# Optimization experiments

Measured on AMD Instinct MI355X. Metric: run time of the kernel, lower is better.

## Reference

```python
import jax, jax.numpy as jnp
import numpy as np

TAU = 2.0      # tau_thr in the source
EPS = 1e-5     # BatchNorm1d default eps
ALPHA = 8.0    # ATan surrogate alpha


@jax.custom_vjp
def atan_spike(x):
    # Heaviside forward, ATan surrogate backward (spikingjelly surrogate.ATan)
    return (x >= 0.0).astype(x.dtype)

def _as_fwd(x):
    return atan_spike(x), x

def _as_bwd(x, g):
    sg = (ALPHA / 2.0) / (1.0 + (jnp.pi / 2.0 * ALPHA * x) ** 2)
    return (g * sg,)

atan_spike.defvjp(_as_fwd, _as_bwd)


def lif(x, thr=1.0):
    # Multi-step LIFNode: v <- v + (x - v)/tau ; spike = H(v - thr);
    # hard reset to v_reset=0 with detach_reset=True.
    def step(v, xt):
        v = v + (xt - v) / TAU
        s = atan_spike(v - thr)
        v = v * (1.0 - jax.lax.stop_gradient(s))
        return v, s
    _, s = jax.lax.scan(step, jnp.zeros_like(x[0]), x)
    return s


def bn(x, p):
    # inference BatchNorm1d over channel dim C of [T,B,C,N]; p = [gamma,beta,mean,var] each [C]
    g, b, m, v = p
    inv = g / jnp.sqrt(v + EPS)
    return x * inv[:, None] + (b - m * inv)[:, None]


def setup_inputs() -> dict:
    key = jax.random.key(0)
    ks = jax.random.split(key, 11)
    T, B, C, H, W = 4, 64, 384, 14, 14
    sc = C ** -0.5
    x = jax.random.normal(ks[0], (T, B, C, H, W), jnp.float32)
    q_w = jax.random.normal(ks[1], (C, C), jnp.float32) * sc
    k_w = jax.random.normal(ks[2], (C, C), jnp.float32) * sc
    v_w = jax.random.normal(ks[3], (C, C), jnp.float32) * sc
    proj_w = jax.random.normal(ks[4], (C, C), jnp.float32) * sc
    proj_b = jax.random.normal(ks[5], (C,), jnp.float32) * 0.02
    def bn_params(k):
        return jax.random.uniform(k, (4, C), jnp.float32, 0.1, 1.0)
    return {
        'x': x, 'q_w': q_w, 'k_w': k_w, 'v_w': v_w,
        'proj_w': proj_w, 'proj_b': proj_b,
        'q_bn_p': bn_params(ks[6]), 'k_bn_p': bn_params(ks[7]),
        'v_bn_p': bn_params(ks[8]), 'p_bn_p': bn_params(ks[9]),
    }


def reference(x, q_w, k_w, v_w, proj_w, proj_b, q_bn_p, k_bn_p, v_bn_p, p_bn_p):
    T, B, C, H, W = x.shape
    nh = 8
    d = C // nh
    N = H * W
    identity = x

    xs = lif(x).reshape(T, B, C, N)  # binary spikes [T,B,C,N]

    def branch(w, p):
        # conv1x1 (C->C) + BN + LIF, then split heads -> [T,B,h,N,d]
        y = bn(jnp.einsum('tbcn,dc->tbdn', xs, w), p)
        s = lif(y)
        return s.reshape(T, B, nh, d, N).transpose(0, 1, 2, 4, 3)

    q = branch(q_w, q_bn_p)
    k = branch(k_w, k_bn_p)
    v = branch(v_w, v_bn_p)

    # unnormalized binary attention (no softmax)
    attn = jnp.einsum('tbhnd,tbhmd->tbhnm', q, k)      # [T,B,h,N,N]
    y = jnp.einsum('tbhnm,tbhmd->tbhnd', attn, v) * 0.125

    y = y.transpose(0, 1, 2, 4, 3).reshape(T, B, C, N)  # merge heads back to C
    y = lif(y, thr=0.5)                                 # attn_lif, v_threshold=0.5

    y = jnp.einsum('tbcn,dc->tbdn', y, proj_w) + proj_b[:, None]
    y = bn(y, p_bn_p)
    return y.reshape(T, B, C, H, W) + identity
```

## Files before the change

kernel.cpp:

```cpp
#include <hip/hip_runtime.h>
#include <hip/hip_bf16.h>

typedef unsigned short u16;
typedef unsigned char  u8;
typedef unsigned int   u32;
typedef unsigned long long u64;
typedef __attribute__((ext_vector_type(8))) short  short8;
typedef __attribute__((ext_vector_type(8))) __bf16 bf16x8;
typedef __attribute__((ext_vector_type(4))) float  f32x4;
typedef __attribute__((ext_vector_type(4))) int    i32x4;

#define DI static __device__ __forceinline__

constexpr int T_ = 4, B_ = 64, C_ = 384, N_ = 196, NH_ = 8, DH_ = 48;
constexpr int J1_ = B_ * N_;
constexpr int J_  = T_ * J1_;
constexpr int K2_ = 2 * C_;
constexpr int M1_ = 3 * C_;

DI u16 f2bf(float x){ __hip_bfloat16 h = __float2bfloat16(x); u16 u; __builtin_memcpy(&u,&h,2); return u; }
DI float bf2f(u16 u){ __hip_bfloat16 h; __builtin_memcpy(&h,&u,2); return __bfloat162float(h); }

DI void gload16(const void* g, void* lds){
  __builtin_amdgcn_global_load_lds((const __attribute__((address_space(1))) u32*)g,
                                   (__attribute__((address_space(3))) u32*)lds, 16, 0, 0);
}
DI bf16x8 ldbf8(const u16* p){ short8 v = *(const short8*)p; return __builtin_bit_cast(bf16x8, v); }
DI int SWZ(int n){ return ((n >> 3) ^ (n >> 5)) & 3; }

__global__ __launch_bounds__(256) void k0_prep(
    const float* __restrict__ qw, const float* __restrict__ kw,
    const float* __restrict__ vw, const float* __restrict__ pw,
    const float* __restrict__ qbn, const float* __restrict__ kbn,
    const float* __restrict__ vbn, const float* __restrict__ pbn,
    u16* __restrict__ A2f, u16* __restrict__ A2pf,
    float* __restrict__ invq, float* __restrict__ betaq,
    float* __restrict__ invp, float* __restrict__ betap)
{
  int id = blockIdx.x * 256 + threadIdx.x;
  const int nAf = M1_ * K2_;
  const int nPf = C_ * K2_;
  if (id < nAf) {
    int tmp = id;
    int e    = tmp & 7;  tmp >>= 3;
    int lane = tmp & 63; tmp >>= 6;
    int ks2  = tmp & 1;  tmp >>= 1;
    int mt   = tmp & 3;  tmp >>= 2;
    int wm   = tmp & 1;  tmp >>= 1;
    int kt   = tmp % 12;
    int bm   = tmp / 12;
    int cc = bm*128 + wm*64 + mt*16 + (lane & 15);
    int k  = kt*64 + ks2*32 + (lane >> 4)*8 + e;
    int br = cc / C_, row = cc % C_;
    const float* w = (br == 0) ? qw : ((br == 1) ? kw : vw);
    float wv = w[row * C_ + (k < C_ ? k : k - C_)];
    u16 hi = f2bf(wv);
    A2f[id] = (k < C_) ? hi : f2bf(__fsub_rn(wv, bf2f(hi)));
  } else if (id < nAf + nPf) {
    int tmp = id - nAf;
    int id2 = tmp;
    int e    = tmp & 7;  tmp >>= 3;
    int lane = tmp & 63; tmp >>= 6;
    int ks2  = tmp & 1;  tmp >>= 1;
    int mt   = tmp & 3;  tmp >>= 2;
    int wm   = tmp & 1;  tmp >>= 1;
    int kt   = tmp % 12;
    int bm   = tmp / 12;
    int cc = bm*128 + wm*64 + mt*16 + (lane & 15);
    int k  = kt*64 + ks2*32 + (lane >> 4)*8 + e;
    float wv = pw[cc * C_ + (k < C_ ? k : k - C_)];
    u16 hi = f2bf(wv);
    A2pf[id2] = (k < C_) ? hi : f2bf(__fsub_rn(wv, bf2f(hi)));
  } else if (id < nAf + nPf + M1_) {
    int c = id - nAf - nPf;
    int br = c / C_, cr = c % C_;
    const float* p = (br == 0) ? qbn : ((br == 1) ? kbn : vbn);
    float g = p[cr], bb = p[C_ + cr], mm = p[2*C_ + cr], vv = p[3*C_ + cr];
    float inv = g / sqrtf(__fadd_rn(vv, 1e-5f));
    invq[c] = inv; betaq[c] = __fsub_rn(bb, __fmul_rn(mm, inv));
  } else if (id < nAf + nPf + M1_ + C_) {
    int c = id - nAf - nPf - M1_;
    float g = pbn[c], bb = pbn[C_ + c], mm = pbn[2*C_ + c], vv = pbn[3*C_ + c];
    float inv = g / sqrtf(__fadd_rn(vv, 1e-5f));
    invp[c] = inv; betap[c] = __fsub_rn(bb, __fmul_rn(mm, inv));
  }
}

__global__ __launch_bounds__(256) void k1_lif_x(const float* __restrict__ x, u16* __restrict__ xs_t)
{
  int b = blockIdx.x / 12, ch = blockIdx.x % 12;
  int c0 = ch * 32;
  __shared__ u16 sp[4 * 32 * 200];
  int tid = threadIdx.x;
  for (int idx = tid; idx < 32 * 49; idx += 256) {
    int ci = idx / 49, n4 = idx % 49;
    float v0 = 0.f, v1 = 0.f, v2 = 0.f, v3 = 0.f;
    for (int t = 0; t < 4; t++) {
      const float4 xv = *reinterpret_cast<const float4*>(
          &x[((size_t)((t*B_ + b)*C_ + c0 + ci))*N_ + n4*4]);
      u16 s0, s1, s2, s3;
      v0 = __fadd_rn(v0, __fmul_rn(__fsub_rn(xv.x, v0), 0.5f)); { bool s = (v0 >= 1.0f); s0 = s ? (u16)0x3F80 : (u16)0; v0 = __fmul_rn(v0, s ? 0.f : 1.f); }
      v1 = __fadd_rn(v1, __fmul_rn(__fsub_rn(xv.y, v1), 0.5f)); { bool s = (v1 >= 1.0f); s1 = s ? (u16)0x3F80 : (u16)0; v1 = __fmul_rn(v1, s ? 0.f : 1.f); }
      v2 = __fadd_rn(v2, __fmul_rn(__fsub_rn(xv.z, v2), 0.5f)); { bool s = (v2 >= 1.0f); s2 = s ? (u16)0x3F80 : (u16)0; v2 = __fmul_rn(v2, s ? 0.f : 1.f); }
      v3 = __fadd_rn(v3, __fmul_rn(__fsub_rn(xv.w, v3), 0.5f)); { bool s = (v3 >= 1.0f); s3 = s ? (u16)0x3F80 : (u16)0; v3 = __fmul_rn(v3, s ? 0.f : 1.f); }
      u64 pk = (u64)s0 | ((u64)s1 << 16) | ((u64)s2 << 32) | ((u64)s3 << 48);
      *reinterpret_cast<u64*>(&sp[(t*32 + ci)*200 + n4*4]) = pk;
    }
  }
  __syncthreads();
  for (int idx = tid; idx < 4 * 8 * N_; idx += 256) {
    int ci4 = idx & 7; int q = idx >> 3; int n = q % N_; int t = q / N_;
    u16 a0 = sp[(t*32 + ci4*4 + 0)*200 + n];
    u16 a1 = sp[(t*32 + ci4*4 + 1)*200 + n];
    u16 a2 = sp[(t*32 + ci4*4 + 2)*200 + n];
    u16 a3 = sp[(t*32 + ci4*4 + 3)*200 + n];
    u64 pk = (u64)a0 | ((u64)a1 << 16) | ((u64)a2 << 32) | ((u64)a3 << 48);
    *reinterpret_cast<u64*>(&xs_t[((size_t)((t*B_ + b)*N_ + n))*C_ + c0 + ci4*4]) = pk;
  }
}

__global__ __launch_bounds__(256, 2) void g1_branch(
    const u16* __restrict__ A2f, const u16* __restrict__ xs_t,
    const float* __restrict__ invq, const float* __restrict__ betaq,
    u8* __restrict__ qs, u8* __restrict__ ks_, u8* __restrict__ vs)
{
  int blk = blockIdx.x;
  int grp = blk / 72, rem = blk % 72;
  int bm = rem >> 3;
  int jt = grp * 8 + (rem & 7);
  if (jt >= 98) return;
  int cc0 = bm * 128;
  int colb = jt * 128;

  __shared__ u16 Bt[128 * 64];

  int tid = threadIdx.x;
  int lane = tid & 63, w = tid >> 6;
  int lr = lane & 15, lg = lane >> 4;
  int rsw = lr & 7;
  int wm = w & 1;
  int mrow = wm * 64, ncol = (w >> 1) * 64;

  float vst[4][4][4];
  #pragma unroll
  for (int a = 0; a < 4; a++)
    #pragma unroll
    for (int bq = 0; bq < 4; bq++)
      #pragma unroll
      for (int r = 0; r < 4; r++) vst[a][bq][r] = 0.f;

  f32x4 acc[4][4];
  bf16x8 af[2][4];

  auto LOADA = [&](int kt2) {
    int wb = (bm * 12 + kt2) * 2 + wm;
    #pragma unroll
    for (int ks2 = 0; ks2 < 2; ks2++)
      #pragma unroll
      for (int mt = 0; mt < 4; mt++)
        af[ks2][mt] = ldbf8(A2f + ((size_t)(((wb * 4 + mt) * 2 + ks2) * 64) + lane) * 8);
  };

  LOADA(0);

  for (int u = 0; u < 48; u++) {
    int t = u / 12, kt = u - t * 12;
    int ckB0 = kt * 64;
    int ckB = (ckB0 >= C_) ? (ckB0 - C_) : ckB0;
    long j0 = (long)t * J1_ + colb;

    #pragma unroll
    for (int i = 0; i < 4; i++) {
      int L0 = tid + i * 256;
      int r = L0 >> 3;
      int c = (L0 & 7) ^ (r & 7);
      gload16(xs_t + (size_t)(j0 + r) * C_ + ckB + c * 8, &Bt[L0 * 8]);
    }

    if (kt == 0) {
      #pragma unroll
      for (int a = 0; a < 4; a++)
        #pragma unroll
        for (int bq = 0; bq < 4; bq++) acc[a][bq] = (f32x4){0.f, 0.f, 0.f, 0.f};
    }
    __syncthreads();

    #pragma unroll
    for (int ks2 = 0; ks2 < 2; ks2++) {
      bf16x8 bfr[4];
      #pragma unroll
      for (int nn = 0; nn < 4; nn++)
        bfr[nn] = ldbf8(&Bt[(ncol + nn*16 + lr)*64 + (((ks2*4 + lg) ^ rsw) * 8)]);
      #pragma unroll
      for (int mt = 0; mt < 4; mt++)
        #pragma unroll
        for (int nn = 0; nn < 4; nn++)
          acc[mt][nn] = __builtin_amdgcn_mfma_f32_16x16x32_bf16(af[ks2][mt], bfr[nn], acc[mt][nn], 0, 0, 0);
    }

    if (u + 1 < 48) {
      int un = u + 1;
      LOADA(un - (un / 12) * 12);
    }

    if (kt == 11) {
      #pragma unroll
      for (int mt = 0; mt < 4; mt++) {
        #pragma unroll
        for (int r = 0; r < 4; r++) {
          int cc = cc0 + mrow + mt*16 + lg*4 + r;
          float inv = invq[cc], beta = betaq[cc];
          int br = cc / C_, c = cc % C_;
          u8* dst = ((br == 0) ? qs : ((br == 1) ? ks_ : vs)) + (size_t)c * J_ + t * J1_ + colb;
          #pragma unroll
          for (int nn = 0; nn < 4; nn++) {
            int col = ncol + nn*16 + lr;
            float yb = __fadd_rn(__fmul_rn(acc[mt][nn][r], inv), beta);
            float v = vst[mt][nn][r];
            v = __fadd_rn(v, __fmul_rn(__fsub_rn(yb, v), 0.5f));
            bool sgl = (v >= 1.0f);
            vst[mt][nn][r] = __fmul_rn(v, sgl ? 0.f : 1.f);
            dst[col] = sgl ? (u8)1 : (u8)0;
          }
        }
      }
    }
    __syncthreads();
  }
}

__global__ __launch_bounds__(256) void k3_attn(
    const u8* __restrict__ qs, const u8* __restrict__ ks_, const u8* __restrict__ vs,
    u16* __restrict__ s2t)
{
  int b = blockIdx.x >> 3, h = blockIdx.x & 7;
  __shared__ __align__(16) signed char qL[208 * 80];
  __shared__ __align__(16) signed char kL[208 * 80];
  __shared__ __align__(16) signed char vL[48 * 272];
  __shared__ __align__(16) signed char aL[4 * 16 * 272];

  int tid = threadIdx.x, lane = tid & 63, w = tid >> 6;
  int lr = lane & 15, lg = lane >> 4;

  for (int i = tid; i < 208*80/4; i += 256) { ((int*)qL)[i] = 0; ((int*)kL)[i] = 0; }
  for (int i = tid; i < 48*272/4; i += 256) ((int*)vL)[i] = 0;
  for (int i = tid; i < 4*16*272/4; i += 256) ((int*)aL)[i] = 0;
  __syncthreads();

  float vst[4][3][4];
  #pragma unroll
  for (int a = 0; a < 4; a++)
    #pragma unroll
    for (int d = 0; d < 3; d++)
      #pragma unroll
      for (int r = 0; r < 4; r++) vst[a][d][r] = 0.f;

  signed char* arow = &aL[w * 16 * 272];
  const i32x4 zero4 = {0, 0, 0, 0};

  for (int t = 0; t < 4; t++) {
    size_t off = (size_t)(t*B_ + b) * N_;
    for (int i = tid; i < 588; i += 256) {
      int dd4 = i / 49, n4 = i - dd4 * 49;
      size_t rb = (size_t)(h*DH_ + dd4*4) * J_ + off + n4*4;
      u32 q0 = *(const u32*)(qs + rb);
      u32 q1 = *(const u32*)(qs + rb + J_);
      u32 q2 = *(const u32*)(qs + rb + 2*(size_t)J_);
      u32 q3 = *(const u32*)(qs + rb + 3*(size_t)J_);
      u32 k0 = *(const u32*)(ks_ + rb);
      u32 k1 = *(const u32*)(ks_ + rb + J_);
      u32 k2 = *(const u32*)(ks_ + rb + 2*(size_t)J_);
      u32 k3 = *(const u32*)(ks_ + rb + 3*(size_t)J_);
      u32 v0 = *(const u32*)(vs + rb);
      u32 v1 = *(const u32*)(vs + rb + J_);
      u32 v2 = *(const u32*)(vs + rb + 2*(size_t)J_);
      u32 v3 = *(const u32*)(vs + rb + 3*(size_t)J_);
      int c16 = dd4 >> 2, bb4 = (dd4 & 3) << 2;
      #pragma unroll
      for (int jj = 0; jj < 4; jj++) {
        u32 tq = ((q0 >> (8*jj)) & 0xFFu) | (((q1 >> (8*jj)) & 0xFFu) << 8)
               | (((q2 >> (8*jj)) & 0xFFu) << 16) | (((q3 >> (8*jj)) & 0xFFu) << 24);
        u32 tk = ((k0 >> (8*jj)) & 0xFFu) | (((k1 >> (8*jj)) & 0xFFu) << 8)
               | (((k2 >> (8*jj)) & 0xFFu) << 16) | (((k3 >> (8*jj)) & 0xFFu) << 24);
        int n = n4*4 + jj;
        int cs = ((c16 ^ SWZ(n)) << 4) + bb4;
        *(u32*)(qL + n*80 + cs) = tq;
        *(u32*)(kL + n*80 + cs) = tk;
      }
      *(u32*)(vL + (dd4*4 + 0)*272 + n4*4) = v0;
      *(u32*)(vL + (dd4*4 + 1)*272 + n4*4) = v1;
      *(u32*)(vL + (dd4*4 + 2)*272 + n4*4) = v2;
      *(u32*)(vL + (dd4*4 + 3)*272 + n4*4) = v3;
    }
    __syncthreads();

    int nslots = (w == 0) ? 4 : 3;
    for (int sl = 0; sl < nslots; sl++) {
      int ni = w + sl * 4;
      int nq = ni*16 + lr;
      i32x4 bq = *reinterpret_cast<const i32x4*>(qL + nq*80 + ((lg ^ SWZ(nq)) << 4));
      for (int mj = 0; mj < 13; mj++) {
        int mk = mj*16 + lr;
        i32x4 ak = *reinterpret_cast<const i32x4*>(kL + mk*80 + ((lg ^ SWZ(mk)) << 4));
        i32x4 d = __builtin_amdgcn_mfma_i32_16x16x64_i8(ak, bq, zero4, 0, 0, 0);
        u32 pk = (u32)d[0] | ((u32)d[1] << 8) | ((u32)d[2] << 16) | ((u32)d[3] << 24);
        *(u32*)(arow + lr*272 + mj*16 + lg*4) = pk;
      }
      #pragma unroll
      for (int di = 0; di < 3; di++) {
        i32x4 acc = zero4;
        #pragma unroll
        for (int ks2 = 0; ks2 < 4; ks2++) {
          i32x4 aa = *reinterpret_cast<const i32x4*>(arow + lr*272 + ks2*64 + lg*16);
          i32x4 bb = *reinterpret_cast<const i32x4*>(vL + (di*16 + lr)*272 + ks2*64 + lg*16);
          acc = __builtin_amdgcn_mfma_i32_16x16x64_i8(aa, bb, acc, 0, 0, 0);
        }
        #pragma unroll
        for (int r = 0; r < 4; r++) {
          int n = ni*16 + lg*4 + r;
          float xv = __fmul_rn((float)acc[r], 0.125f);
          float v = vst[sl][di][r];
          v = __fadd_rn(v, __fmul_rn(__fsub_rn(xv, v), 0.5f));
          bool s = (v >= 0.5f);
          vst[sl][di][r] = __fmul_rn(v, s ? 0.f : 1.f);
          if (n < N_)
            s2t[((size_t)((t*B_ + b)*N_ + n))*C_ + h*DH_ + di*16 + lr] = s ? (u16)0x3F80 : (u16)0;
        }
      }
    }
    __syncthreads();
  }
}

__global__ __launch_bounds__(256, 2) void g2_proj(
    const u16* __restrict__ A2pf, const u16* __restrict__ s2t,
    const float* __restrict__ invp, const float* __restrict__ betap,
    const float* __restrict__ pb, const float* __restrict__ x,
    float* __restrict__ out)
{
  int blk = blockIdx.x;
  int grp = blk / 24, rem = blk % 24;
  int bm = rem >> 3;
  int bn = grp * 8 + (rem & 7);
  int cc0 = bm * 128, j0 = bn * 128;

  __shared__ u16 Bt[128 * 64];

  int tid = threadIdx.x;
  int lane = tid & 63, w = tid >> 6;
  int lr = lane & 15, lg = lane >> 4;
  int rsw = lr & 7;
  int wm = w & 1;
  int mrow = wm * 64, ncol = (w >> 1) * 64;

  f32x4 acc[4][4];
  #pragma unroll
  for (int a = 0; a < 4; a++)
    #pragma unroll
    for (int bq = 0; bq < 4; bq++) acc[a][bq] = (f32x4){0.f, 0.f, 0.f, 0.f};

  bf16x8 af[2][4];
  auto LOADA = [&](int kt2) {
    int wb = (bm * 12 + kt2) * 2 + wm;
    #pragma unroll
    for (int ks2 = 0; ks2 < 2; ks2++)
      #pragma unroll
      for (int mt = 0; mt < 4; mt++)
        af[ks2][mt] = ldbf8(A2pf + ((size_t)(((wb * 4 + mt) * 2 + ks2) * 64) + lane) * 8);
  };

  LOADA(0);

  for (int kt = 0; kt < 12; kt++) {
    int ckB0 = kt * 64;
    int ckB = (ckB0 >= C_) ? (ckB0 - C_) : ckB0;
    #pragma unroll
    for (int i = 0; i < 4; i++) {
      int L0 = tid + i * 256;
      int r = L0 >> 3;
      int c = (L0 & 7) ^ (r & 7);
      gload16(s2t + (size_t)(j0 + r) * C_ + ckB + c * 8, &Bt[L0 * 8]);
    }
    __syncthreads();

    #pragma unroll
    for (int ks2 = 0; ks2 < 2; ks2++) {
      bf16x8 bfr[4];
      #pragma unroll
      for (int nn = 0; nn < 4; nn++)
        bfr[nn] = ldbf8(&Bt[(ncol + nn*16 + lr)*64 + (((ks2*4 + lg) ^ rsw) * 8)]);
      #pragma unroll
      for (int mt = 0; mt < 4; mt++)
        #pragma unroll
        for (int nn = 0; nn < 4; nn++)
          acc[mt][nn] = __builtin_amdgcn_mfma_f32_16x16x32_bf16(af[ks2][mt], bfr[nn], acc[mt][nn], 0, 0, 0);
    }

    if (kt < 11) LOADA(kt + 1);
    __syncthreads();
  }

  #pragma unroll
  for (int mt = 0; mt < 4; mt++) {
    #pragma unroll
    for (int r = 0; r < 4; r++) {
      int cc = cc0 + mrow + mt*16 + lg*4 + r;
      float inv = invp[cc], beta = betap[cc], pbv = pb[cc];
      #pragma unroll
      for (int nn = 0; nn < 4; nn++) {
        int j = j0 + ncol + nn*16 + lr;
        float y = __fadd_rn(acc[mt][nn][r], pbv);
        float o = __fadd_rn(__fmul_rn(y, inv), beta);
        int jq = j / N_, n = j % N_;
        size_t addr = ((size_t)jq * C_ + cc) * N_ + n;
        out[addr] = __fadd_rn(o, x[addr]);
      }
    }
  }
}

extern "C" void kernel_launch(void* const* d_in, const int* in_sizes, int n_in,
                              void* d_out, int out_size, void* d_ws, size_t ws_size,
                              hipStream_t stream)
{
  (void)in_sizes; (void)n_in; (void)out_size; (void)ws_size;
  const float* x   = (const float*)d_in[0];
  const float* qw  = (const float*)d_in[1];
  const float* kw  = (const float*)d_in[2];
  const float* vw  = (const float*)d_in[3];
  const float* pw  = (const float*)d_in[4];
  const float* pbv = (const float*)d_in[5];
  const float* qbn = (const float*)d_in[6];
  const float* kbn = (const float*)d_in[7];
  const float* vbn = (const float*)d_in[8];
  const float* pbn = (const float*)d_in[9];

  char* ws = (char*)d_ws;
  u16*   A2f   = (u16*)  (ws + 0);
  u16*   A2pf  = (u16*)  (ws + 1769472);
  float* invq  = (float*)(ws + 2359296);
  float* betaq = (float*)(ws + 2363904);
  float* invp  = (float*)(ws + 2368512);
  float* betap = (float*)(ws + 2370048);
  u16*   xs_t  = (u16*)  (ws + 2371584);
  u16*   s2t   = xs_t;
  u8*    qs    = (u8*)   (ws + 40906752);
  u8*    ks    = (u8*)   (ws + 60174336);
  u8*    vs    = (u8*)   (ws + 79441920);

  k0_prep<<<4614, 256, 0, stream>>>(qw, kw, vw, pw, qbn, kbn, vbn, pbn,
                                    A2f, A2pf, invq, betaq, invp, betap);
  k1_lif_x<<<768, 256, 0, stream>>>(x, xs_t);
  g1_branch<<<936, 256, 0, stream>>>(A2f, xs_t, invq, betaq, qs, ks, vs);
  k3_attn<<<512, 256, 0, stream>>>(qs, ks, vs, s2t);
  g2_proj<<<1176, 256, 0, stream>>>(A2pf, s2t, invp, betap, pbv, x, (float*)d_out);
}
```

Baseline: 294.1 us.

## Write Q/K spikes in per-head token-major layout and load MFMA fragments directly

The branch GEMM epilogue now writes Q and K spikes into a per-(t,b,head) page laid out token-major with 48 bytes per token, packing four channels per 32-bit store. The attention kernel then reads Q/K MFMA fragments straight from global memory instead of transposing and staging them through swizzled LDS, which removes that LDS staging pass and its transposition arithmetic. The prep kernel zero-fills the padding rows of each page. The cost is uncached global reads inside the inner attention loop and more prep work.

```diff
diff --git a/kernel.cpp b/kernel.cpp
--- a/kernel.cpp
+++ b/kernel.cpp
@@ -17,6 +17,7 @@
 constexpr int J_  = T_ * J1_;
 constexpr int K2_ = 2 * C_;
 constexpr int M1_ = 3 * C_;
+constexpr int PGE_ = 208 * 48;
 
 DI u16 f2bf(float x){ __hip_bfloat16 h = __float2bfloat16(x); u16 u; __builtin_memcpy(&u,&h,2); return u; }
 DI float bf2f(u16 u){ __hip_bfloat16 h; __builtin_memcpy(&h,&u,2); return __bfloat162float(h); }
@@ -26,7 +27,6 @@
                                    (__attribute__((address_space(3))) u32*)lds, 16, 0, 0);
 }
 DI bf16x8 ldbf8(const u16* p){ short8 v = *(const short8*)p; return __builtin_bit_cast(bf16x8, v); }
-DI int SWZ(int n){ return ((n >> 3) ^ (n >> 5)) & 3; }
 
 __global__ __launch_bounds__(256) void k0_prep(
     const float* __restrict__ qw, const float* __restrict__ kw,
@@ -35,11 +35,14 @@
     const float* __restrict__ vbn, const float* __restrict__ pbn,
     u16* __restrict__ A2f, u16* __restrict__ A2pf,
     float* __restrict__ invq, float* __restrict__ betaq,
-    float* __restrict__ invp, float* __restrict__ betap)
+    float* __restrict__ invp, float* __restrict__ betap,
+    u8* __restrict__ qt, u8* __restrict__ kt_)
 {
   int id = blockIdx.x * 256 + threadIdx.x;
   const int nAf = M1_ * K2_;
   const int nPf = C_ * K2_;
+  const int base1 = nAf + nPf + M1_ + C_;
+  const int nPad = 2048 * 144;
   if (id < nAf) {
     int tmp = id;
     int e    = tmp & 7;  tmp >>= 3;
@@ -78,11 +81,19 @@
     float g = p[cr], bb = p[C_ + cr], mm = p[2*C_ + cr], vv = p[3*C_ + cr];
     float inv = g / sqrtf(__fadd_rn(vv, 1e-5f));
     invq[c] = inv; betaq[c] = __fsub_rn(bb, __fmul_rn(mm, inv));
-  } else if (id < nAf + nPf + M1_ + C_) {
+  } else if (id < base1) {
     int c = id - nAf - nPf - M1_;
     float g = pbn[c], bb = pbn[C_ + c], mm = pbn[2*C_ + c], vv = pbn[3*C_ + c];
     float inv = g / sqrtf(__fadd_rn(vv, 1e-5f));
     invp[c] = inv; betap[c] = __fsub_rn(bb, __fmul_rn(mm, inv));
+  } else if (id < base1 + nPad) {
+    int id3 = id - base1;
+    int p = id3 / 144, rr = (id3 % 144) / 12, uu = id3 % 12;
+    *(u32*)(qt + (size_t)p * PGE_ + (196 + rr) * 48 + uu * 4) = 0u;
+  } else if (id < base1 + 2 * nPad) {
+    int id3 = id - base1 - nPad;
+    int p = id3 / 144, rr = (id3 % 144) / 12, uu = id3 % 12;
+    *(u32*)(kt_ + (size_t)p * PGE_ + (196 + rr) * 48 + uu * 4) = 0u;
   }
 }
 
@@ -122,7 +133,7 @@
 __global__ __launch_bounds__(256, 2) void g1_branch(
     const u16* __restrict__ A2f, const u16* __restrict__ xs_t,
     const float* __restrict__ invq, const float* __restrict__ betaq,
-    u8* __restrict__ qs, u8* __restrict__ ks_, u8* __restrict__ vs)
+    u8* __restrict__ qt, u8* __restrict__ kt_, u8* __restrict__ vs)
 {
   int blk = blockIdx.x;
   int grp = blk / 72, rem = blk % 72;
@@ -140,6 +151,7 @@
   int rsw = lr & 7;
   int wm = w & 1;
   int mrow = wm * 64, ncol = (w >> 1) * 64;
+  int brw = (cc0 + mrow) / C_;
 
   float vst[4][4][4];
   #pragma unroll
@@ -204,23 +216,53 @@
     }
 
     if (kt == 11) {
-      #pragma unroll
-      for (int mt = 0; mt < 4; mt++) {
-        #pragma unroll
-        for (int r = 0; r < 4; r++) {
-          int cc = cc0 + mrow + mt*16 + lg*4 + r;
-          float inv = invq[cc], beta = betaq[cc];
-          int br = cc / C_, c = cc % C_;
-          u8* dst = ((br == 0) ? qs : ((br == 1) ? ks_ : vs)) + (size_t)c * J_ + t * J1_ + colb;
+      if (brw == 2) {
+        #pragma unroll
+        for (int mt = 0; mt < 4; mt++) {
+          #pragma unroll
+          for (int r = 0; r < 4; r++) {
+            int cc = cc0 + mrow + mt*16 + lg*4 + r;
+            float inv = invq[cc], beta = betaq[cc];
+            int c = cc - 2 * C_;
+            u8* dst = vs + (size_t)c * J_ + t * J1_ + colb;
+            #pragma unroll
+            for (int nn = 0; nn < 4; nn++) {
+              int col = ncol + nn*16 + lr;
+              float yb = __fadd_rn(__fmul_rn(acc[mt][nn][r], inv), beta);
+              float v = vst[mt][nn][r];
+              v = __fadd_rn(v, __fmul_rn(__fsub_rn(yb, v), 0.5f));
+              bool sgl = (v >= 1.0f);
+              vst[mt][nn][r] = __fmul_rn(v, sgl ? 0.f : 1.f);
+              dst[col] = sgl ? (u8)1 : (u8)0;
+            }
+          }
+        }
+      } else {
+        u8* baseb = brw ? kt_ : qt;
+        #pragma unroll
+        for (int mt = 0; mt < 4; mt++) {
+          int ccb = cc0 + mrow + mt*16 + lg*4;
+          float invv[4], betav[4];
+          #pragma unroll
+          for (int r = 0; r < 4; r++) { invv[r] = invq[ccb + r]; betav[r] = betaq[ccb + r]; }
+          int c = ccb - brw * C_;
+          int h = c / DH_, dd0 = c % DH_;
           #pragma unroll
           for (int nn = 0; nn < 4; nn++) {
-            int col = ncol + nn*16 + lr;
-            float yb = __fadd_rn(__fmul_rn(acc[mt][nn][r], inv), beta);
-            float v = vst[mt][nn][r];
-            v = __fadd_rn(v, __fmul_rn(__fsub_rn(yb, v), 0.5f));
-            bool sgl = (v >= 1.0f);
-            vst[mt][nn][r] = __fmul_rn(v, sgl ? 0.f : 1.f);
-            dst[col] = sgl ? (u8)1 : (u8)0;
+            int col = colb + ncol + nn*16 + lr;
+            u32 bidx = ((u32)col * 85599u) >> 24;
+            int n = col - (int)bidx * 196;
+            u32 pk = 0;
+            #pragma unroll
+            for (int r = 0; r < 4; r++) {
+              float yb = __fadd_rn(__fmul_rn(acc[mt][nn][r], invv[r]), betav[r]);
+              float v = vst[mt][nn][r];
+              v = __fadd_rn(v, __fmul_rn(__fsub_rn(yb, v), 0.5f));
+              bool sgl = (v >= 1.0f);
+              vst[mt][nn][r] = __fmul_rn(v, sgl ? 0.f : 1.f);
+              pk |= (sgl ? 1u : 0u) << (8 * r);
+            }
+            *(u32*)(baseb + (size_t)((t*B_ + (int)bidx)*NH_ + h) * PGE_ + n*48 + dd0) = pk;
           }
         }
       }
@@ -230,20 +272,17 @@
 }
 
 __global__ __launch_bounds__(256) void k3_attn(
-    const u8* __restrict__ qs, const u8* __restrict__ ks_, const u8* __restrict__ vs,
+    const u8* __restrict__ qt, const u8* __restrict__ kt_, const u8* __restrict__ vs,
     u16* __restrict__ s2t)
 {
   int b = blockIdx.x >> 3, h = blockIdx.x & 7;
-  __shared__ __align__(16) signed char qL[208 * 80];
-  __shared__ __align__(16) signed char kL[208 * 80];
-  __shared__ __align__(16) signed char vL[48 * 272];
+  __shared__ __align__(16) signed char vL[48 * 304];
   __shared__ __align__(16) signed char aL[4 * 16 * 272];
 
   int tid = threadIdx.x, lane = tid & 63, w = tid >> 6;
   int lr = lane & 15, lg = lane >> 4;
 
-  for (int i = tid; i < 208*80/4; i += 256) { ((int*)qL)[i] = 0; ((int*)kL)[i] = 0; }
-  for (int i = tid; i < 48*272/4; i += 256) ((int*)vL)[i] = 0;
+  for (int i = tid; i < 48*304/4; i += 256) ((int*)vL)[i] = 0;
   for (int i = tid; i < 4*16*272/4; i += 256) ((int*)aL)[i] = 0;
   __syncthreads();
 
@@ -260,49 +299,25 @@
 
   for (int t = 0; t < 4; t++) {
     size_t off = (size_t)(t*B_ + b) * N_;
-    for (int i = tid; i < 588; i += 256) {
-      int dd4 = i / 49, n4 = i - dd4 * 49;
-      size_t rb = (size_t)(h*DH_ + dd4*4) * J_ + off + n4*4;
-      u32 q0 = *(const u32*)(qs + rb);
-      u32 q1 = *(const u32*)(qs + rb + J_);
-      u32 q2 = *(const u32*)(qs + rb + 2*(size_t)J_);
-      u32 q3 = *(const u32*)(qs + rb + 3*(size_t)J_);
-      u32 k0 = *(const u32*)(ks_ + rb);
-      u32 k1 = *(const u32*)(ks_ + rb + J_);
-      u32 k2 = *(const u32*)(ks_ + rb + 2*(size_t)J_);
-      u32 k3 = *(const u32*)(ks_ + rb + 3*(size_t)J_);
-      u32 v0 = *(const u32*)(vs + rb);
-      u32 v1 = *(const u32*)(vs + rb + J_);
-      u32 v2 = *(const u32*)(vs + rb + 2*(size_t)J_);
-      u32 v3 = *(const u32*)(vs + rb + 3*(size_t)J_);
-      int c16 = dd4 >> 2, bb4 = (dd4 & 3) << 2;
-      #pragma unroll
-      for (int jj = 0; jj < 4; jj++) {
-        u32 tq = ((q0 >> (8*jj)) & 0xFFu) | (((q1 >> (8*jj)) & 0xFFu) << 8)
-               | (((q2 >> (8*jj)) & 0xFFu) << 16) | (((q3 >> (8*jj)) & 0xFFu) << 24);
-        u32 tk = ((k0 >> (8*jj)) & 0xFFu) | (((k1 >> (8*jj)) & 0xFFu) << 8)
-               | (((k2 >> (8*jj)) & 0xFFu) << 16) | (((k3 >> (8*jj)) & 0xFFu) << 24);
-        int n = n4*4 + jj;
-        int cs = ((c16 ^ SWZ(n)) << 4) + bb4;
-        *(u32*)(qL + n*80 + cs) = tq;
-        *(u32*)(kL + n*80 + cs) = tk;
-      }
-      *(u32*)(vL + (dd4*4 + 0)*272 + n4*4) = v0;
-      *(u32*)(vL + (dd4*4 + 1)*272 + n4*4) = v1;
-      *(u32*)(vL + (dd4*4 + 2)*272 + n4*4) = v2;
-      *(u32*)(vL + (dd4*4 + 3)*272 + n4*4) = v3;
-    }
-    __syncthreads();
-
+    for (int i = tid; i < 48 * 49; i += 256) {
+      int dd = i / 49, n4 = i - dd * 49;
+      u32 vv = *(const u32*)(vs + (size_t)(h*DH_ + dd) * J_ + off + n4*4);
+      *(u32*)(vL + dd*304 + n4*4) = vv;
+    }
+    __syncthreads();
+
+    size_t pb = (size_t)((t*B_ + b)*NH_ + h) * PGE_;
     int nslots = (w == 0) ? 4 : 3;
     for (int sl = 0; sl < nslots; sl++) {
       int ni = w + sl * 4;
       int nq = ni*16 + lr;
-      i32x4 bq = *reinterpret_cast<const i32x4*>(qL + nq*80 + ((lg ^ SWZ(nq)) << 4));
+      i32x4 afr = zero4;
+      if (lg < 3) afr = *reinterpret_cast<const i32x4*>(qt + pb + (size_t)nq*48 + lg*16);
       for (int mj = 0; mj < 13; mj++) {
         int mk = mj*16 + lr;
-        i32x4 ak = *reinterpret_cast<const i32x4*>(kL + mk*80 + ((lg ^ SWZ(mk)) << 4));
-        i32x4 d = __builtin_amdgcn_mfma_i32_16x16x64_i8(ak, bq, zero4, 0, 0, 0);
+        i32x4 ak = zero4;
+        if (lg < 3) ak = *reinterpret_cast<const i32x4*>(kt_ + pb + (size_t)mk*48 + lg*16);
+        i32x4 d = __builtin_amdgcn_mfma_i32_16x16x64_i8(ak, afr, zero4, 0, 0, 0);
         u32 pk = (u32)d[0] | ((u32)d[1] << 8) | ((u32)d[2] << 16) | ((u32)d[3] << 24);
         *(u32*)(arow + lr*272 + mj*16 + lg*4) = pk;
       }
@@ -312,7 +327,7 @@
         #pragma unroll
         for (int ks2 = 0; ks2 < 4; ks2++) {
           i32x4 aa = *reinterpret_cast<const i32x4*>(arow + lr*272 + ks2*64 + lg*16);
-          i32x4 bb = *reinterpret_cast<const i32x4*>(vL + (di*16 + lr)*272 + ks2*64 + lg*16);
+          i32x4 bb = *reinterpret_cast<const i32x4*>(vL + (di*16 + lr)*304 + ks2*64 + lg*16);
           acc = __builtin_amdgcn_mfma_i32_16x16x64_i8(aa, bb, acc, 0, 0, 0);
         }
         #pragma unroll
@@ -444,14 +459,14 @@
   float* betap = (float*)(ws + 2370048);
   u16*   xs_t  = (u16*)  (ws + 2371584);
   u16*   s2t   = xs_t;
-  u8*    qs    = (u8*)   (ws + 40906752);
-  u8*    ks    = (u8*)   (ws + 60174336);
-  u8*    vs    = (u8*)   (ws + 79441920);
-
-  k0_prep<<<4614, 256, 0, stream>>>(qw, kw, vw, pw, qbn, kbn, vbn, pbn,
-                                    A2f, A2pf, invq, betaq, invp, betap);
+  u8*    qt    = (u8*)   (ws + 40906752);
+  u8*    kt_   = (u8*)   (ws + 61353984);
+  u8*    vs    = (u8*)   (ws + 81801216);
+
+  k0_prep<<<6918, 256, 0, stream>>>(qw, kw, vw, pw, qbn, kbn, vbn, pbn,
+                                    A2f, A2pf, invq, betaq, invp, betap, qt, kt_);
   k1_lif_x<<<768, 256, 0, stream>>>(x, xs_t);
-  g1_branch<<<936, 256, 0, stream>>>(A2f, xs_t, invq, betaq, qs, ks, vs);
-  k3_attn<<<512, 256, 0, stream>>>(qs, ks, vs, s2t);
+  g1_branch<<<936, 256, 0, stream>>>(A2f, xs_t, invq, betaq, qt, kt_, vs);
+  k3_attn<<<512, 256, 0, stream>>>(qt, kt_, vs, s2t);
   g2_proj<<<1176, 256, 0, stream>>>(A2pf, s2t, invp, betap, pbv, x, (float*)d_out);
 }
```

After: 418.8 us. +42.4%, slower.
